# Optimization experiments

Measured on AMD Instinct MI355X. Metric: run time of the kernel, lower is better.

The kernel has to match this reference:

```python
import jax, jax.numpy as jnp
import numpy as np

B, C, H, W = 2, 3, 512, 512
P = 16
D = 768
NH = 12
DEPTH = 12
MLP = 4
HP, WP = H // P, W // P
N = HP * WP
DH = D // NH          # 64
ROPE_BASE = 100.0     # from pos_embed='RoPE100'


def _ln(x, w, b, eps):
    m = jnp.mean(x, -1, keepdims=True)
    v = jnp.mean((x - m) ** 2, -1, keepdims=True)
    return (x - m) * jax.lax.rsqrt(v + eps) * w + b


def _rope_tables(maxpos, d):
    inv = 1.0 / (ROPE_BASE ** (jnp.arange(0, d, 2, dtype=jnp.float32) / d))
    f = jnp.arange(maxpos, dtype=jnp.float32)[:, None] * inv[None, :]
    f = jnp.concatenate([f, f], -1)  # [maxpos, d]
    return jnp.cos(f), jnp.sin(f)


def _rot_half(x):
    x1, x2 = jnp.split(x, 2, -1)
    return jnp.concatenate([-x2, x1], -1)


def _rope2d(t, pos, cos, sin):
    # t: [B,NH,N,DH]; pos: [B,N,2] (y,x). First half of DH rotated by y, second by x.
    def rot1d(tok, p):
        c = cos[p][:, None]  # [B,1,N,DH//2]
        s = sin[p][:, None]
        return tok * c + _rot_half(tok) * s
    ty, tx = jnp.split(t, 2, -1)
    return jnp.concatenate([rot1d(ty, pos[..., 0]), rot1d(tx, pos[..., 1])], -1)


def _forward(image, patch_w, patch_b, ln1_w, ln1_b, qkv_w, qkv_b, proj_w, proj_b,
             ln2_w, ln2_b, fc1_w, fc1_b, fc2_w, fc2_b, encn_w, encn_b):
    # patch embed: conv stride=patch, flatten row-major (y-major, matching cartesian_prod(y,x))
    x = jax.lax.conv_general_dilated(image, patch_w, (P, P), 'VALID',
                                     dimension_numbers=('NCHW', 'OIHW', 'NCHW'))
    x = (x + patch_b[None, :, None, None]).reshape(B, D, N).transpose(0, 2, 1)  # [B,N,D]
    yy, xx = jnp.meshgrid(jnp.arange(HP), jnp.arange(WP), indexing='ij')
    pos = jnp.broadcast_to(jnp.stack([yy, xx], -1).reshape(N, 2), (B, N, 2))
    cos, sin = _rope_tables(max(HP, WP), DH // 2)
    scale = DH ** -0.5
    for i in range(DEPTH):
        h = _ln(x, ln1_w[i], ln1_b[i], 1e-5)
        qkv = (h @ qkv_w[i].T + qkv_b[i]).reshape(B, N, 3, NH, DH).transpose(2, 0, 3, 1, 4)
        q, k, v = qkv[0], qkv[1], qkv[2]  # [B,NH,N,DH]
        q = _rope2d(q, pos, cos, sin)
        k = _rope2d(k, pos, cos, sin)
        att = jax.nn.softmax(jnp.einsum('bhqd,bhkd->bhqk', q, k) * scale, -1)
        o = jnp.einsum('bhqk,bhkd->bhqd', att, v).transpose(0, 2, 1, 3).reshape(B, N, D)
        x = x + o @ proj_w[i].T + proj_b[i]
        h = _ln(x, ln2_w[i], ln2_b[i], 1e-5)
        h = jax.nn.gelu(h @ fc1_w[i].T + fc1_b[i], approximate=False)
        x = x + h @ fc2_w[i].T + fc2_b[i]
    x = _ln(x, encn_w, encn_b, 1e-6)
    return x, pos


def setup_inputs() -> dict:
    key = jax.random.key(0)
    ks = jax.random.split(key, 8)
    s = 0.02
    dff = MLP * D
    return {
        "image": jax.random.normal(ks[0], (B, C, H, W), jnp.float32),
        "true_shape": jnp.full((B, 2), H, jnp.int32),
        "patch_w": jax.random.normal(ks[1], (D, C, P, P), jnp.float32) * s,
        "patch_b": jnp.zeros((D,), jnp.float32),
        "ln1_w": jnp.ones((DEPTH, D), jnp.float32),
        "ln1_b": jnp.zeros((DEPTH, D), jnp.float32),
        "qkv_w": jax.random.normal(ks[2], (DEPTH, 3 * D, D), jnp.float32) * s,
        "qkv_b": jnp.zeros((DEPTH, 3 * D), jnp.float32),
        "proj_w": jax.random.normal(ks[3], (DEPTH, D, D), jnp.float32) * s,
        "proj_b": jnp.zeros((DEPTH, D), jnp.float32),
        "ln2_w": jnp.ones((DEPTH, D), jnp.float32),
        "ln2_b": jnp.zeros((DEPTH, D), jnp.float32),
        "fc1_w": jax.random.normal(ks[4], (DEPTH, dff, D), jnp.float32) * s,
        "fc1_b": jnp.zeros((DEPTH, dff), jnp.float32),
        "fc2_w": jax.random.normal(ks[5], (DEPTH, D, dff), jnp.float32) * s,
        "fc2_b": jnp.zeros((DEPTH, D), jnp.float32),
        "encn_w": jnp.ones((D,), jnp.float32),
        "encn_b": jnp.zeros((D,), jnp.float32),
    }


def reference(image, true_shape, patch_w, patch_b, ln1_w, ln1_b, qkv_w, qkv_b,
              proj_w, proj_b, ln2_w, ln2_b, fc1_w, fc1_b, fc2_w, fc2_b,
              encn_w, encn_b):
    # true_shape assumed full-resolution (all images H x W); positions are static grid
    return _forward(image, patch_w, patch_b, ln1_w, ln1_b, qkv_w, qkv_b, proj_w,
                    proj_b, ln2_w, ln2_b, fc1_w, fc1_b, fc2_w, fc2_b, encn_w, encn_b)
```

## Files before the change

### kernel.cpp

```cpp
#include <hip/hip_runtime.h>
#include <hip/hip_bf16.h>
#include <stdint.h>

typedef unsigned short u16;
typedef __attribute__((ext_vector_type(8))) short bf16x8;
typedef __attribute__((ext_vector_type(4))) float f32x4;
typedef __attribute__((ext_vector_type(4))) u16 u16x4;
typedef __attribute__((ext_vector_type(8))) u16 u16x8;
typedef __attribute__((ext_vector_type(4))) uint32_t u32x4;

__device__ __forceinline__ u16 f2bf(float f) {
  union { float f; uint32_t u; } v; v.f = f;
  uint32_t u = v.u + 0x7FFFu + ((v.u >> 16) & 1u);
  return (u16)(u >> 16);
}
__device__ __forceinline__ float bf2f(u16 h) {
  union { uint32_t u; float f; } v; v.u = ((uint32_t)h) << 16;
  return v.f;
}

__device__ __forceinline__ int xcd_swz(int hw, int n) {
  return (n & 7) ? hw : (hw & 7) * (n >> 3) + (hw >> 3);
}

__device__ __forceinline__ void gload_lds16(const void* g, void* l) {
  __builtin_amdgcn_global_load_lds(
      (const __attribute__((address_space(1))) void*)g,
      (__attribute__((address_space(3))) void*)l, 16, 0, 0);
}

__global__ __launch_bounds__(256) void cast_f32_bf16(const float* __restrict__ src,
                                                     u16* __restrict__ dst, int n4) {
  int i = blockIdx.x * 256 + threadIdx.x;
  if (i < n4) {
    float4 v = ((const float4*)src)[i];
    u16x4 o; o.x = f2bf(v.x); o.y = f2bf(v.y); o.z = f2bf(v.z); o.w = f2bf(v.w);
    ((u16x4*)dst)[i] = o;
  }
}

__global__ __launch_bounds__(256)
void cast8_all(const float* __restrict__ s0, const float* __restrict__ s1,
               const float* __restrict__ s2, const float* __restrict__ s3,
               const float* __restrict__ s4,
               u16* __restrict__ d0, u16* __restrict__ d1, u16* __restrict__ d2,
               u16* __restrict__ d3, u16* __restrict__ d4,
               long n0, long n1, long n2, long n3, long n4) {
  long i = (long)blockIdx.x * 256 + threadIdx.x;
  const float* s; u16* d; long off;
  if (i < n0) { s = s0; d = d0; off = i; }
  else if (i < n0 + n1) { s = s1; d = d1; off = i - n0; }
  else if (i < n0 + n1 + n2) { s = s2; d = d2; off = i - n0 - n1; }
  else if (i < n0 + n1 + n2 + n3) { s = s3; d = d3; off = i - n0 - n1 - n2; }
  else if (i < n0 + n1 + n2 + n3 + n4) { s = s4; d = d4; off = i - n0 - n1 - n2 - n3; }
  else return;
  float4 a = ((const float4*)s)[off * 2];
  float4 b = ((const float4*)s)[off * 2 + 1];
  u16x8 o;
  o[0] = f2bf(a.x); o[1] = f2bf(a.y); o[2] = f2bf(a.z); o[3] = f2bf(a.w);
  o[4] = f2bf(b.x); o[5] = f2bf(b.y); o[6] = f2bf(b.z); o[7] = f2bf(b.w);
  ((u16x8*)d)[off] = o;
}

__global__ __launch_bounds__(256) void im2col_kernel(const float* __restrict__ img,
                                                     u16* __restrict__ out) {
  int f = blockIdx.x * 256 + threadIdx.x;
  int row = blockIdx.y;
  int b = row >> 10, n = row & 1023, py = n >> 5, px = n & 31;
  int c = f >> 8, rem = f & 255, i = rem >> 4, j = rem & 15;
  float v = img[(((size_t)b * 3 + c) * 512 + py * 16 + i) * 512 + px * 16 + j];
  out[(size_t)row * 768 + f] = f2bf(v);
}

template <int EPI, int XGX, int XGY, int XGZ>
__global__ __launch_bounds__(256, 2)
void gemm_bt(const u16* __restrict__ A, const u16* __restrict__ W,
             const float* __restrict__ bias, void* __restrict__ outp,
             int M, int N, int K, int lda, int ldw) {
  constexpr int AB = 128 * 128;
  constexpr int BB = 128 * 128;
  constexpr int BUF = AB + BB;
  constexpr int LOADS = BUF / 4096;
  __shared__ char smem[2 * BUF];
  const int tid = threadIdx.x;
  const int lane = tid & 63;
  const int w = tid >> 6;
  const int qr = lane & 15;
  const int kg = lane >> 4;
  const int gx = gridDim.x, gy = gridDim.y;
  const int hw = blockIdx.x + gx * (blockIdx.y + gy * blockIdx.z);
  const int xcd = hw & 7, i = hw >> 3;
  const int sx = gx / XGX, sy = gy / XGY;
  const int cx = xcd % XGX, cy = (xcd / XGX) % XGY, cz = xcd / (XGX * XGY);
  const int bn = cx * sx + i % sx;
  const int rr_ = i / sx;
  const int bm = cy * sy + rr_ % sy;
  const int bz = cz * (gridDim.z / XGZ) + rr_ / sy;
  const int wr = (w >> 1) * 64;
  const int wc = (w & 1) * 64;
  const size_t arow0 = (size_t)bm * 128;
  const size_t wrow0 = (size_t)bn * 128;
  const u16* Ab = A + (size_t)bz * K;
  const u16* Wb = W + (size_t)bz * K;

  f32x4 acc[4][4] = {};

  auto stage = [&](int buf, int kt) {
    char* As = smem + buf * BUF;
    char* Ws = As + AB;
#pragma unroll
    for (int r = 0; r < 4; ++r) {
      int o = r * 4096 + tid * 16;
      int row = o >> 7;
      int lc = (o & 127) ^ ((row & 7) << 4);
      gload_lds16(Ab + (arow0 + row) * lda + kt + (lc >> 1), As + o);
    }
#pragma unroll
    for (int r = 0; r < 4; ++r) {
      int o = r * 4096 + tid * 16;
      int row = o >> 7;
      int lc = (o & 127) ^ ((row & 7) << 4);
      gload_lds16(Wb + (wrow0 + row) * ldw + kt + (lc >> 1), Ws + o);
    }
  };

  const int nt = K >> 6;
  stage(0, 0);
  stage(1, 64);
  for (int t = 0; t < nt; ++t) {
    if (t + 1 < nt) {
      asm volatile("s_waitcnt vmcnt(%0)" :: "i"(LOADS) : "memory");
    } else {
      asm volatile("s_waitcnt vmcnt(0)" ::: "memory");
    }
    __builtin_amdgcn_s_barrier();
    const char* As = smem + (t & 1) * BUF;
    const char* Ws = As + AB;
    bf16x8 af[2][4], bfr[2][4];
#pragma unroll
    for (int m = 0; m < 4; ++m) {
      int row = wr + m * 16 + qr;
      af[0][m] = *(const bf16x8*)(As + row * 128 + ((kg * 16) ^ ((row & 7) << 4)));
    }
#pragma unroll
    for (int n = 0; n < 4; ++n) {
      int row = wc + n * 16 + qr;
      bfr[0][n] = *(const bf16x8*)(Ws + row * 128 + ((kg * 16) ^ ((row & 7) << 4)));
    }
    __builtin_amdgcn_sched_barrier(0);
#pragma unroll
    for (int m = 0; m < 4; ++m) {
      int row = wr + m * 16 + qr;
      af[1][m] = *(const bf16x8*)(As + row * 128 + ((64 + kg * 16) ^ ((row & 7) << 4)));
    }
#pragma unroll
    for (int n = 0; n < 4; ++n) {
      int row = wc + n * 16 + qr;
      bfr[1][n] = *(const bf16x8*)(Ws + row * 128 + ((64 + kg * 16) ^ ((row & 7) << 4)));
    }
    asm volatile("s_waitcnt lgkmcnt(8)" ::: "memory");
    __builtin_amdgcn_sched_barrier(0);
#pragma unroll
    for (int m = 0; m < 4; ++m)
#pragma unroll
      for (int n = 0; n < 4; ++n)
        acc[m][n] = __builtin_amdgcn_mfma_f32_16x16x32_bf16(af[0][m], bfr[0][n], acc[m][n], 0, 0, 0);
    asm volatile("s_waitcnt lgkmcnt(0)" ::: "memory");
    __builtin_amdgcn_sched_barrier(0);
    __builtin_amdgcn_s_barrier();
    if (t + 2 < nt) stage(t & 1, (t + 2) << 6);
#pragma unroll
    for (int m = 0; m < 4; ++m)
#pragma unroll
      for (int n = 0; n < 4; ++n)
        acc[m][n] = __builtin_amdgcn_mfma_f32_16x16x32_bf16(af[1][m], bfr[1][n], acc[m][n], 0, 0, 0);
  }

  const int r0 = bm * 128 + wr + kg * 4;
  const int c0 = bn * 128 + wc + qr;
  if constexpr (EPI == 4) {
    const int headbase = bn * 128 + wc;
    const bool isqk = headbase < 1536;
    const float linv = exp2f(-0.41524101186092122f * (float)qr);
    u16* outb = (u16*)outp;
#pragma unroll
    for (int m = 0; m < 4; ++m) {
#pragma unroll
      for (int j = 0; j < 4; ++j) {
        int row = r0 + m * 16 + j;
        int tok = row & 1023;
        float vs[4];
#pragma unroll
        for (int n = 0; n < 4; ++n) vs[n] = acc[m][n][j] + bias[c0 + n * 16];
        if (isqk) {
          float sy, cy, sxv, cxv;
          __sincosf((float)(tok >> 5) * linv, &sy, &cy);
          __sincosf((float)(tok & 31) * linv, &sxv, &cxv);
          float a0 = vs[0], a1 = vs[1], a2 = vs[2], a3 = vs[3];
          vs[0] = a0 * cy - a1 * sy;
          vs[1] = a1 * cy + a0 * sy;
          vs[2] = a2 * cxv - a3 * sxv;
          vs[3] = a3 * cxv + a2 * sxv;
        }
#pragma unroll
        for (int n = 0; n < 4; ++n)
          outb[(size_t)row * N + c0 + n * 16] = f2bf(vs[n]);
      }
    }
  } else if constexpr (EPI == 5) {
    u16* outb = (u16*)outp + (size_t)bz * M * N;
#pragma unroll
    for (int m = 0; m < 4; ++m)
#pragma unroll
      for (int j = 0; j < 4; ++j) {
        int row = r0 + m * 16 + j;
#pragma unroll
        for (int n = 0; n < 4; ++n)
          outb[(size_t)row * N + c0 + n * 16] = f2bf(acc[m][n][j]);
      }
  } else {
    u16* outb = (u16*)outp;
#pragma unroll
    for (int m = 0; m < 4; ++m)
#pragma unroll
      for (int j = 0; j < 4; ++j) {
        int row = r0 + m * 16 + j;
#pragma unroll
        for (int n = 0; n < 4; ++n) {
          int col = c0 + n * 16;
          float v = acc[m][n][j] + bias[col];
          v = 0.5f * v * (1.0f + erff(v * 0.70710678118654752f));
          outb[(size_t)row * N + col] = f2bf(v);
        }
      }
  }
}

template <int FINAL>
__global__ __launch_bounds__(192)
void fuse_red_ln(const u16* __restrict__ parts, const float* __restrict__ bias,
                 const u16* __restrict__ resid, u16* __restrict__ xout,
                 void* __restrict__ lnout, const float* __restrict__ lw,
                 const float* __restrict__ lb, float eps) {
  if (FINAL && blockIdx.x >= 2048) {
    int i = (blockIdx.x - 2048) * 192 + threadIdx.x;
    if (i < 4096) {
      int c = i & 1, n = (i >> 1) & 1023;
      ((float*)lnout)[(size_t)2048 * 768 + i] = (float)(c ? (n & 31) : (n >> 5));
    }
    return;
  }
  const int row = blockIdx.x, t = threadIdx.x;
  const int c0 = t * 4;
  constexpr size_t MN = (size_t)2048 * 768;
  const u16x4 pa = *(const u16x4*)(parts + (size_t)row * 768 + c0);
  const u16x4 pb = *(const u16x4*)(parts + MN + (size_t)row * 768 + c0);
  const f32x4 bi = *(const f32x4*)(bias + c0);
  f32x4 v;
#pragma unroll
  for (int j = 0; j < 4; ++j) v[j] = bf2f(pa[j]) + bf2f(pb[j]) + bi[j];
  if (resid) {
    const u16x4 rv = *(const u16x4*)(resid + (size_t)row * 768 + c0);
#pragma unroll
    for (int j = 0; j < 4; ++j) v[j] += bf2f(rv[j]);
  }
  if (xout) {
    u16x4 xo;
#pragma unroll
    for (int j = 0; j < 4; ++j) xo[j] = f2bf(v[j]);
    *(u16x4*)(xout + (size_t)row * 768 + c0) = xo;
#pragma unroll
    for (int j = 0; j < 4; ++j) v[j] = bf2f(xo[j]);
  }
  float s = (v[0] + v[1]) + (v[2] + v[3]);
  float sq = (v[0] * v[0] + v[1] * v[1]) + (v[2] * v[2] + v[3] * v[3]);
#pragma unroll
  for (int m = 1; m < 64; m <<= 1) {
    s += __shfl_xor(s, m);
    sq += __shfl_xor(sq, m);
  }
  __shared__ float red[6];
  int wv = t >> 6;
  if ((t & 63) == 0) { red[wv] = s; red[3 + wv] = sq; }
  __syncthreads();
  s = red[0] + red[1] + red[2];
  sq = red[3] + red[4] + red[5];
  float mean = s * (1.0f / 768.0f);
  float var = sq * (1.0f / 768.0f) - mean * mean;
  float rstd = rsqrtf(var + eps);
  const f32x4 lwv = *(const f32x4*)(lw + c0);
  const f32x4 lbv = *(const f32x4*)(lb + c0);
  if (FINAL) {
    f32x4 o;
#pragma unroll
    for (int j = 0; j < 4; ++j) o[j] = (v[j] - mean) * rstd * lwv[j] + lbv[j];
    *(f32x4*)((float*)lnout + (size_t)row * 768 + c0) = o;
  } else {
    u16x4 o;
#pragma unroll
    for (int j = 0; j < 4; ++j) o[j] = f2bf((v[j] - mean) * rstd * lwv[j] + lbv[j]);
    *(u16x4*)((u16*)lnout + (size_t)row * 768 + c0) = o;
  }
}

__global__ __launch_bounds__(128)
void attn_kernel(const u16* __restrict__ qkv, u16* __restrict__ o) {
  __shared__ char smem[32768];
  const int tid = threadIdx.x, lane = tid & 63, w = tid >> 6;
  const int qr = lane & 15, kg = lane >> 4;
  const bool kgodd = (kg & 1) != 0;
  const int lid = xcd_swz(blockIdx.x, gridDim.x);
  const int qb = lid & 31, bh = lid >> 5;
  const int b = bh / 12, h = bh % 12;
  const int qrow0 = qb * 32 + w * 16;
  const u16* kvb = qkv + (size_t)b * 1024 * 2304;

  bf16x8 aq[2];
  {
    const u16* qbase = qkv + ((size_t)(b * 1024 + qrow0 + qr)) * 2304 + h * 64;
    aq[0] = *(const bf16x8*)(qbase + kg * 8);
    aq[1] = *(const bf16x8*)(qbase + 32 + kg * 8);
#pragma unroll
    for (int r = 0; r < 2; ++r)
#pragma unroll
      for (int e = 0; e < 8; ++e)
        aq[r][e] = (short)f2bf(bf2f((u16)aq[r][e]) * 0.125f);
  }
  f32x4 oacc[4] = {};
  float lsum = 0.f;

  const int kvp = tid >> 3, dg = tid & 7;
  bf16x8 va[2], vb[2];
  auto issueV = [&](int kt) {
#pragma unroll
    for (int rr = 0; rr < 2; ++rr) {
      int p = rr * 16 + kvp;
      const u16* vsrc = kvb + ((size_t)(kt * 64 + 2 * p)) * 2304 + 1536 + h * 64 + dg * 8;
      va[rr] = *(const bf16x8*)vsrc;
      vb[rr] = *(const bf16x8*)(vsrc + 2304);
    }
  };
  auto issueK = [&](int kt, int bsel) {
    char* Ks = smem + bsel * 8192;
#pragma unroll
    for (int r = 0; r < 4; ++r) {
      int off = r * 2048 + tid * 16;
      int kv = off >> 7;
      int db = (off ^ ((kv & 7) << 4)) & 127;
      gload_lds16(kvb + ((size_t)(kt * 64 + kv)) * 2304 + 768 + h * 64 + (db >> 1), Ks + off);
    }
  };
  auto writeV = [&](int bsel) {
    char* Vt = smem + 16384 + bsel * 8192;
#pragma unroll
    for (int rr = 0; rr < 2; ++rr) {
      int p = rr * 16 + kvp;
#pragma unroll
      for (int j = 0; j < 8; ++j) {
        int d = dg * 8 + j;
        uint32_t pk = (uint32_t)(u16)va[rr][j] | ((uint32_t)(u16)vb[rr][j] << 16);
        *(uint32_t*)(Vt + ((d * 128 + p * 4) ^ (((dg ^ j) & 7) << 4))) = pk;
      }
    }
  };

  issueV(0);
  issueK(0, 0);
  writeV(0);

  for (int kt = 0; kt < 16; ++kt) {
    const int c = kt & 1;
    asm volatile("s_waitcnt vmcnt(0) lgkmcnt(0)" ::: "memory");
    __builtin_amdgcn_s_barrier();
    if (kt + 1 < 16) { issueV(kt + 1); issueK(kt + 1, c ^ 1); }

    const char* Ks = smem + c * 8192;
    const char* Vt = smem + 16384 + c * 8192;

    bf16x8 bk[2][4];
#pragma unroll
    for (int n = 0; n < 4; ++n) {
      int row = n * 16 + qr;
      bk[0][n] = *(const bf16x8*)(Ks + ((row * 128 + kg * 16) ^ ((row & 7) << 4)));
    }
    __builtin_amdgcn_sched_barrier(0);
#pragma unroll
    for (int n = 0; n < 4; ++n) {
      int row = n * 16 + qr;
      bk[1][n] = *(const bf16x8*)(Ks + ((row * 128 + 64 + kg * 16) ^ ((row & 7) << 4)));
    }
    f32x4 sa[4] = {};
    asm volatile("s_waitcnt lgkmcnt(4)" ::: "memory");
    __builtin_amdgcn_sched_barrier(0);
    __builtin_amdgcn_s_setprio(1);
#pragma unroll
    for (int n = 0; n < 4; ++n)
      sa[n] = __builtin_amdgcn_mfma_f32_16x16x32_bf16(bk[0][n], aq[0], sa[n], 0, 0, 0);
    asm volatile("s_waitcnt lgkmcnt(0)" ::: "memory");
    __builtin_amdgcn_sched_barrier(0);
#pragma unroll
    for (int n = 0; n < 4; ++n)
      sa[n] = __builtin_amdgcn_mfma_f32_16x16x32_bf16(bk[1][n], aq[1], sa[n], 0, 0, 0);
    __builtin_amdgcn_s_setprio(0);

    float pv[4][4];
    float ts = 0.f;
#pragma unroll
    for (int n = 0; n < 4; ++n)
#pragma unroll
      for (int j = 0; j < 4; ++j) {
        pv[n][j] = __expf(sa[n][j]);
        ts += pv[n][j];
      }
    lsum += ts;

    if (kt + 1 < 16) writeV(c ^ 1);

    bf16x8 vf[2][4];
#pragma unroll
    for (int ks = 0; ks < 2; ++ks)
#pragma unroll
      for (int n = 0; n < 4; ++n) {
        int d = n * 16 + qr;
        vf[ks][n] = *(const bf16x8*)(Vt + ((d * 128 + ks * 64 + kg * 16) ^ ((((d >> 3) ^ (d & 7)) & 7) << 4)));
      }

    uint32_t pk0[4], pk1[4];
#pragma unroll
    for (int n = 0; n < 4; ++n) {
      asm("v_cvt_pk_bf16_f32 %0, %1, %2" : "=v"(pk0[n]) : "v"(pv[n][0]), "v"(pv[n][1]));
      asm("v_cvt_pk_bf16_f32 %0, %1, %2" : "=v"(pk1[n]) : "v"(pv[n][2]), "v"(pv[n][3]));
    }
    bf16x8 pb[2];
#pragma unroll
    for (int ks = 0; ks < 2; ++ks) {
      uint32_t A0 = pk0[ks * 2], B0 = pk0[ks * 2 + 1];
      uint32_t A1 = pk1[ks * 2], B1 = pk1[ks * 2 + 1];
      asm("v_permlane32_swap_b32 %0, %1" : "+v"(A0), "+v"(B0));
      asm("v_permlane32_swap_b32 %0, %1" : "+v"(A1), "+v"(B1));
      uint32_t sA0 = (uint32_t)__shfl_xor((int)A0, 16);
      uint32_t sA1 = (uint32_t)__shfl_xor((int)A1, 16);
      uint32_t sB0 = (uint32_t)__shfl_xor((int)B0, 16);
      uint32_t sB1 = (uint32_t)__shfl_xor((int)B1, 16);
      u32x4 dd;
      dd.x = kgodd ? sB0 : A0;
      dd.y = kgodd ? sB1 : A1;
      dd.z = kgodd ? B0 : sA0;
      dd.w = kgodd ? B1 : sA1;
      pb[ks] = __builtin_bit_cast(bf16x8, dd);
    }

    __builtin_amdgcn_s_setprio(1);
#pragma unroll
    for (int ks = 0; ks < 2; ++ks)
#pragma unroll
      for (int n = 0; n < 4; ++n)
        oacc[n] = __builtin_amdgcn_mfma_f32_16x16x32_bf16(vf[ks][n], pb[ks], oacc[n], 0, 0, 0);
    __builtin_amdgcn_s_setprio(0);
  }
  lsum += __shfl_xor(lsum, 16);
  lsum += __shfl_xor(lsum, 32);
  float inv = 1.0f / lsum;
  const size_t rowg = (size_t)(b * 1024 + qrow0 + qr);
#pragma unroll
  for (int n = 0; n < 4; ++n) {
    u16x4 ov;
#pragma unroll
    for (int j = 0; j < 4; ++j) ov[j] = f2bf(oacc[n][j] * inv);
    *(u16x4*)(o + rowg * 768 + h * 64 + n * 16 + kg * 4) = ov;
  }
}

extern "C" void kernel_launch(void* const* d_in, const int* in_sizes, int n_in,
                              void* d_out, int out_size, void* d_ws, size_t ws_size,
                              hipStream_t stream) {
  const float* image  = (const float*)d_in[0];
  const float* patch_w = (const float*)d_in[2];
  const float* patch_b = (const float*)d_in[3];
  const float* ln1_w = (const float*)d_in[4];
  const float* ln1_b = (const float*)d_in[5];
  const float* qkv_w = (const float*)d_in[6];
  const float* qkv_b = (const float*)d_in[7];
  const float* proj_w = (const float*)d_in[8];
  const float* proj_b = (const float*)d_in[9];
  const float* ln2_w = (const float*)d_in[10];
  const float* ln2_b = (const float*)d_in[11];
  const float* fc1_w = (const float*)d_in[12];
  const float* fc1_b = (const float*)d_in[13];
  const float* fc2_w = (const float*)d_in[14];
  const float* fc2_b = (const float*)d_in[15];
  const float* encn_w = (const float*)d_in[16];
  const float* encn_b = (const float*)d_in[17];

  char* ws = (char*)d_ws;
  size_t off = 0;
  auto alloc = [&](size_t bytes) {
    char* pr = ws + off;
    off += (bytes + 255) & ~(size_t)255;
    return pr;
  };

  u16* x      = (u16*)alloc((size_t)2048 * 768 * 2);
  u16* hbuf   = (u16*)alloc((size_t)2048 * 768 * 2);
  u16* qkvb   = (u16*)alloc((size_t)2048 * 2304 * 2);
  u16* obuf   = (u16*)alloc((size_t)2048 * 768 * 2);
  u16* h2     = (u16*)alloc((size_t)2048 * 3072 * 2);
  u16* wpb    = (u16*)alloc((size_t)768 * 768 * 2);
  u16* parts  = (u16*)alloc((size_t)2 * 2048 * 768 * 2);

  const size_t wq_n = (size_t)12 * 2304 * 768;
  const size_t wp_n = (size_t)12 * 768 * 768;
  const size_t w1_n = (size_t)12 * 3072 * 768;
  const size_t w2_n = (size_t)12 * 3072 * 768;
  bool upfront = (off + 2 * (wq_n + wp_n + w1_n + w2_n) + (1u << 20)) <= ws_size;

  u16 *wq, *wp, *w1, *w2;
  if (upfront) {
    wq = (u16*)alloc(wq_n * 2);
    wp = (u16*)alloc(wp_n * 2);
    w1 = (u16*)alloc(w1_n * 2);
    w2 = (u16*)alloc(w2_n * 2);
  } else {
    wq = (u16*)alloc((size_t)2304 * 768 * 2);
    wp = (u16*)alloc((size_t)768 * 768 * 2);
    w1 = (u16*)alloc((size_t)3072 * 768 * 2);
    w2 = (u16*)alloc((size_t)3072 * 768 * 2);
  }

  auto cast = [&](const float* s, u16* d, size_t n) {
    int n4 = (int)(n / 4);
    cast_f32_bf16<<<(n4 + 255) / 256, 256, 0, stream>>>(s, d, n4);
  };

  if (upfront) {
    long n0 = (long)(wq_n / 8), n1 = (long)(wp_n / 8), n2 = (long)(w1_n / 8),
         n3 = (long)(w2_n / 8), n4 = (long)(768 * 768 / 8);
    long ntot = n0 + n1 + n2 + n3 + n4;
    cast8_all<<<(int)((ntot + 255) / 256), 256, 0, stream>>>(
        qkv_w, proj_w, fc1_w, fc2_w, patch_w, wq, wp, w1, w2, wpb,
        n0, n1, n2, n3, n4);
  } else {
    cast(patch_w, wpb, (size_t)768 * 768);
  }

  im2col_kernel<<<dim3(3, 2048), 256, 0, stream>>>(image, hbuf);
  gemm_bt<5, 2, 2, 2><<<dim3(6, 16, 2), 256, 0, stream>>>(hbuf, wpb, nullptr, parts, 2048, 768, 384, 768, 768);
  fuse_red_ln<0><<<2048, 192, 0, stream>>>(parts, patch_b, nullptr, x, hbuf, ln1_w, ln1_b, 1e-5f);

  for (int L = 0; L < 12; ++L) {
    u16 *wqL, *wpL, *w1L, *w2L;
    if (upfront) {
      wqL = wq + (size_t)L * 2304 * 768;
      wpL = wp + (size_t)L * 768 * 768;
      w1L = w1 + (size_t)L * 3072 * 768;
      w2L = w2 + (size_t)L * 3072 * 768;
    } else {
      cast(qkv_w + (size_t)L * 2304 * 768, wq, (size_t)2304 * 768);
      cast(proj_w + (size_t)L * 768 * 768, wp, (size_t)768 * 768);
      cast(fc1_w + (size_t)L * 3072 * 768, w1, (size_t)3072 * 768);
      cast(fc2_w + (size_t)L * 768 * 3072, w2, (size_t)3072 * 768);
      wqL = wq; wpL = wp; w1L = w1; w2L = w2;
    }
    gemm_bt<4, 2, 4, 1><<<dim3(18, 16), 256, 0, stream>>>(hbuf, wqL, qkv_b + L * 2304, qkvb, 2048, 2304, 768, 768, 768);
    attn_kernel<<<768, 128, 0, stream>>>(qkvb, obuf);
    gemm_bt<5, 2, 2, 2><<<dim3(6, 16, 2), 256, 0, stream>>>(obuf, wpL, nullptr, parts, 2048, 768, 384, 768, 768);
    fuse_red_ln<0><<<2048, 192, 0, stream>>>(parts, proj_b + L * 768, x, x, hbuf,
                                             ln2_w + L * 768, ln2_b + L * 768, 1e-5f);
    gemm_bt<1, 2, 4, 1><<<dim3(24, 16), 256, 0, stream>>>(hbuf, w1L, fc1_b + L * 3072, h2, 2048, 3072, 768, 768, 768);
    gemm_bt<5, 2, 2, 2><<<dim3(6, 16, 2), 256, 0, stream>>>(h2, w2L, nullptr, parts, 2048, 768, 1536, 3072, 3072);
    if (L < 11) {
      fuse_red_ln<0><<<2048, 192, 0, stream>>>(parts, fc2_b + L * 768, x, x, hbuf,
                                               ln1_w + (L + 1) * 768, ln1_b + (L + 1) * 768, 1e-5f);
    } else {
      fuse_red_ln<1><<<2070, 192, 0, stream>>>(parts, fc2_b + L * 768, x, nullptr, (float*)d_out,
                                               encn_w, encn_b, 1e-6f);
    }
  }
}
```

Baseline: 1.231 ms.

## Load attention K fragments directly to registers and widen weight cast to 16 elements

```diff
diff --git a/kernel.cpp b/kernel.cpp
--- a/kernel.cpp
+++ b/kernel.cpp
@@ -40,12 +40,12 @@
 }
 
 __global__ __launch_bounds__(256)
-void cast8_all(const float* __restrict__ s0, const float* __restrict__ s1,
-               const float* __restrict__ s2, const float* __restrict__ s3,
-               const float* __restrict__ s4,
-               u16* __restrict__ d0, u16* __restrict__ d1, u16* __restrict__ d2,
-               u16* __restrict__ d3, u16* __restrict__ d4,
-               long n0, long n1, long n2, long n3, long n4) {
+void cast16_all(const float* __restrict__ s0, const float* __restrict__ s1,
+                const float* __restrict__ s2, const float* __restrict__ s3,
+                const float* __restrict__ s4,
+                u16* __restrict__ d0, u16* __restrict__ d1, u16* __restrict__ d2,
+                u16* __restrict__ d3, u16* __restrict__ d4,
+                long n0, long n1, long n2, long n3, long n4) {
   long i = (long)blockIdx.x * 256 + threadIdx.x;
   const float* s; u16* d; long off;
   if (i < n0) { s = s0; d = d0; off = i; }
@@ -54,12 +54,18 @@
   else if (i < n0 + n1 + n2 + n3) { s = s3; d = d3; off = i - n0 - n1 - n2; }
   else if (i < n0 + n1 + n2 + n3 + n4) { s = s4; d = d4; off = i - n0 - n1 - n2 - n3; }
   else return;
-  float4 a = ((const float4*)s)[off * 2];
-  float4 b = ((const float4*)s)[off * 2 + 1];
-  u16x8 o;
-  o[0] = f2bf(a.x); o[1] = f2bf(a.y); o[2] = f2bf(a.z); o[3] = f2bf(a.w);
-  o[4] = f2bf(b.x); o[5] = f2bf(b.y); o[6] = f2bf(b.z); o[7] = f2bf(b.w);
-  ((u16x8*)d)[off] = o;
+  const f32x4* sp = (const f32x4*)s + off * 4;
+  f32x4 a = __builtin_nontemporal_load(sp);
+  f32x4 b = __builtin_nontemporal_load(sp + 1);
+  f32x4 c = __builtin_nontemporal_load(sp + 2);
+  f32x4 e = __builtin_nontemporal_load(sp + 3);
+  u16x8 o1, o2;
+#pragma unroll
+  for (int j = 0; j < 4; ++j) { o1[j] = f2bf(a[j]); o1[4 + j] = f2bf(b[j]); }
+#pragma unroll
+  for (int j = 0; j < 4; ++j) { o2[j] = f2bf(c[j]); o2[4 + j] = f2bf(e[j]); }
+  ((u16x8*)d)[off * 2] = o1;
+  ((u16x8*)d)[off * 2 + 1] = o2;
 }
 
 __global__ __launch_bounds__(256) void im2col_kernel(const float* __restrict__ img,
@@ -305,7 +311,7 @@
 
 __global__ __launch_bounds__(128)
 void attn_kernel(const u16* __restrict__ qkv, u16* __restrict__ o) {
-  __shared__ char smem[32768];
+  __shared__ char smem[16384];
   const int tid = threadIdx.x, lane = tid & 63, w = tid >> 6;
   const int qr = lane & 15, kg = lane >> 4;
   const bool kgodd = (kg & 1) != 0;
@@ -340,18 +346,17 @@
       vb[rr] = *(const bf16x8*)(vsrc + 2304);
     }
   };
-  auto issueK = [&](int kt, int bsel) {
-    char* Ks = smem + bsel * 8192;
-#pragma unroll
-    for (int r = 0; r < 4; ++r) {
-      int off = r * 2048 + tid * 16;
-      int kv = off >> 7;
-      int db = (off ^ ((kv & 7) << 4)) & 127;
-      gload_lds16(kvb + ((size_t)(kt * 64 + kv)) * 2304 + 768 + h * 64 + (db >> 1), Ks + off);
-    }
+  auto loadK = [&](int kt, bf16x8 (&bk)[2][4]) {
+#pragma unroll
+    for (int ks = 0; ks < 2; ++ks)
+#pragma unroll
+      for (int n = 0; n < 4; ++n) {
+        int row = kt * 64 + n * 16 + qr;
+        bk[ks][n] = *(const bf16x8*)(kvb + (size_t)row * 2304 + 768 + h * 64 + ks * 32 + kg * 8);
+      }
   };
   auto writeV = [&](int bsel) {
-    char* Vt = smem + 16384 + bsel * 8192;
+    char* Vt = smem + bsel * 8192;
 #pragma unroll
     for (int rr = 0; rr < 2; ++rr) {
       int p = rr * 16 + kvp;
@@ -364,43 +369,25 @@
     }
   };
 
+  bf16x8 bkA[2][4], bkB[2][4];
+  loadK(0, bkA);
   issueV(0);
-  issueK(0, 0);
   writeV(0);
 
-  for (int kt = 0; kt < 16; ++kt) {
+  auto body = [&](int kt, bf16x8 (&cur)[2][4], bf16x8 (&nxt)[2][4]) {
     const int c = kt & 1;
-    asm volatile("s_waitcnt vmcnt(0) lgkmcnt(0)" ::: "memory");
+    asm volatile("s_waitcnt lgkmcnt(0)" ::: "memory");
     __builtin_amdgcn_s_barrier();
-    if (kt + 1 < 16) { issueV(kt + 1); issueK(kt + 1, c ^ 1); }
-
-    const char* Ks = smem + c * 8192;
-    const char* Vt = smem + 16384 + c * 8192;
-
-    bf16x8 bk[2][4];
-#pragma unroll
-    for (int n = 0; n < 4; ++n) {
-      int row = n * 16 + qr;
-      bk[0][n] = *(const bf16x8*)(Ks + ((row * 128 + kg * 16) ^ ((row & 7) << 4)));
-    }
-    __builtin_amdgcn_sched_barrier(0);
-#pragma unroll
-    for (int n = 0; n < 4; ++n) {
-      int row = n * 16 + qr;
-      bk[1][n] = *(const bf16x8*)(Ks + ((row * 128 + 64 + kg * 16) ^ ((row & 7) << 4)));
-    }
+    asm volatile("s_waitcnt vmcnt(0)" ::: "memory");
+    if (kt + 1 < 16) { issueV(kt + 1); loadK(kt + 1, nxt); }
+
     f32x4 sa[4] = {};
-    asm volatile("s_waitcnt lgkmcnt(4)" ::: "memory");
-    __builtin_amdgcn_sched_barrier(0);
     __builtin_amdgcn_s_setprio(1);
 #pragma unroll
-    for (int n = 0; n < 4; ++n)
-      sa[n] = __builtin_amdgcn_mfma_f32_16x16x32_bf16(bk[0][n], aq[0], sa[n], 0, 0, 0);
-    asm volatile("s_waitcnt lgkmcnt(0)" ::: "memory");
-    __builtin_amdgcn_sched_barrier(0);
-#pragma unroll
-    for (int n = 0; n < 4; ++n)
-      sa[n] = __builtin_amdgcn_mfma_f32_16x16x32_bf16(bk[1][n], aq[1], sa[n], 0, 0, 0);
+    for (int ks = 0; ks < 2; ++ks)
+#pragma unroll
+      for (int n = 0; n < 4; ++n)
+        sa[n] = __builtin_amdgcn_mfma_f32_16x16x32_bf16(cur[ks][n], aq[ks], sa[n], 0, 0, 0);
     __builtin_amdgcn_s_setprio(0);
 
     float pv[4][4];
@@ -416,6 +403,7 @@
 
     if (kt + 1 < 16) writeV(c ^ 1);
 
+    const char* Vt = smem + c * 8192;
     bf16x8 vf[2][4];
 #pragma unroll
     for (int ks = 0; ks < 2; ++ks)
@@ -457,7 +445,13 @@
       for (int n = 0; n < 4; ++n)
         oacc[n] = __builtin_amdgcn_mfma_f32_16x16x32_bf16(vf[ks][n], pb[ks], oacc[n], 0, 0, 0);
     __builtin_amdgcn_s_setprio(0);
-  }
+  };
+
+  for (int k8 = 0; k8 < 8; ++k8) {
+    body(2 * k8, bkA, bkB);
+    body(2 * k8 + 1, bkB, bkA);
+  }
+
   lsum += __shfl_xor(lsum, 16);
   lsum += __shfl_xor(lsum, 32);
   float inv = 1.0f / lsum;
@@ -533,10 +527,10 @@
   };
 
   if (upfront) {
-    long n0 = (long)(wq_n / 8), n1 = (long)(wp_n / 8), n2 = (long)(w1_n / 8),
-         n3 = (long)(w2_n / 8), n4 = (long)(768 * 768 / 8);
+    long n0 = (long)(wq_n / 16), n1 = (long)(wp_n / 16), n2 = (long)(w1_n / 16),
+         n3 = (long)(w2_n / 16), n4 = (long)(768 * 768 / 16);
     long ntot = n0 + n1 + n2 + n3 + n4;
-    cast8_all<<<(int)((ntot + 255) / 256), 256, 0, stream>>>(
+    cast16_all<<<(int)((ntot + 255) / 256), 256, 0, stream>>>(
         qkv_w, proj_w, fc1_w, fc2_w, patch_w, wq, wp, w1, w2, wpb,
         n0, n1, n2, n3, n4);
   } else {
```

After: 1.299 ms. 5.6% more time.
